# Kernel optimization log

Measured on AMD Instinct MI355X. Metric: run time of the kernel, lower is better.

Reference implementation:

```python
import math
import jax, jax.numpy as jnp
import numpy as np

H = 8
C_HIDDEN = 32
C_Q = 256


def setup_inputs() -> dict:
    key = jax.random.key(0)
    ks = jax.random.split(key, 9)
    B, S, Q, K = 1, 128, 256, 256
    q_x = jax.random.normal(ks[0], (B, S, Q, C_Q), dtype=jnp.float32)
    kv_x = jax.random.normal(ks[1], (B, S, K, C_Q), dtype=jnp.float32)
    bias1 = jax.random.normal(ks[2], (B, S, 1, 1, K), dtype=jnp.float32)
    bias2 = jax.random.normal(ks[3], (B, 1, H, Q, K), dtype=jnp.float32)
    scale = 1.0 / math.sqrt(C_Q)
    wq = jax.random.normal(ks[4], (H * C_HIDDEN, C_Q), dtype=jnp.float32) * scale
    wk = jax.random.normal(ks[5], (H * C_HIDDEN, C_Q), dtype=jnp.float32) * scale
    wv = jax.random.normal(ks[6], (H * C_HIDDEN, C_Q), dtype=jnp.float32) * scale
    wg = jax.random.normal(ks[7], (H * C_HIDDEN, C_Q), dtype=jnp.float32) * scale
    wo = jax.random.normal(ks[8], (C_Q, H * C_HIDDEN), dtype=jnp.float32) * scale
    return {"q_x": q_x, "kv_x": kv_x, "bias1": bias1, "bias2": bias2,
            "wq": wq, "wk": wk, "wv": wv, "wg": wg, "wo": wo}


def _split_heads(x):
    # [..., L, H*c] -> [..., H, L, c]
    y = x.reshape(x.shape[:-1] + (H, C_HIDDEN))
    return jnp.moveaxis(y, -2, -3)


def reference(q_x, kv_x, bias1, bias2, wq, wk, wv, wg, wo):
    # QKV projections (no bias), per-head split, scale q by 1/sqrt(c_hidden)
    q = _split_heads(q_x @ wq.T) / math.sqrt(C_HIDDEN)   # [B,S,H,Q,c]
    k = _split_heads(kv_x @ wk.T)                         # [B,S,H,K,c]
    v = _split_heads(kv_x @ wv.T)                         # [B,S,H,K,c]
    # attention logits with additive biases folded in
    a = jnp.einsum('...hqc,...hkc->...hqk', q, k) + bias1 + bias2
    a = jax.nn.softmax(a, axis=-1)
    o = jnp.einsum('...hqk,...hkc->...hqc', a, v)         # [B,S,H,Q,c]
    o = jnp.moveaxis(o, -3, -2)                           # [B,S,Q,H,c]
    # sigmoid gating from query data
    g = jax.nn.sigmoid(q_x @ wg.T)                        # [B,S,Q,H*c]
    g = g.reshape(g.shape[:-1] + (H, C_HIDDEN))
    o = o * g
    o = o.reshape(o.shape[:-2] + (H * C_HIDDEN,))         # flatten heads
    return o @ wo.T                                       # [B,S,Q,C_Q]
```

## Files before the change

kernel.cpp:

```cpp
#include <hip/hip_runtime.h>
#include <math.h>

#define S_DIM 128
#define H_DIM 8
#define M_TOT (S_DIM * 256)

typedef unsigned short ushort_t;
typedef unsigned int   uint32;
typedef __bf16  v8bf  __attribute__((ext_vector_type(8)));
typedef float   v4f   __attribute__((ext_vector_type(4)));

__device__ inline ushort_t f2b(float x) {
    unsigned int u = __float_as_uint(x);
    u += 0x7fffu + ((u >> 16) & 1u);
    return (ushort_t)(u >> 16);
}
__device__ inline float b2f(ushort_t h) {
    return __uint_as_float(((unsigned int)h) << 16);
}

#define GLDS16(gp, lp) __builtin_amdgcn_global_load_lds( \
    (const __attribute__((address_space(1))) void*)(gp), \
    (__attribute__((address_space(3))) void*)(lp), 16, 0, 0)

__global__ __launch_bounds__(256) void split_x(
    const float* __restrict__ xq, const float* __restrict__ xkv,
    ushort_t* __restrict__ hi, ushort_t* __restrict__ lo)
{
    const size_t BUF4 = (size_t)M_TOT * 64;
    const float* src = blockIdx.y ? xkv : xq;
    size_t base = (size_t)blockIdx.y * BUF4;
    int i = blockIdx.x * 256 + threadIdx.x;
    float4 v = ((const float4*)src)[i];
    ushort4 h, l;
    h.x = f2b(v.x); l.x = f2b(v.x - b2f(h.x));
    h.y = f2b(v.y); l.y = f2b(v.y - b2f(h.y));
    h.z = f2b(v.z); l.z = f2b(v.z - b2f(h.z));
    h.w = f2b(v.w); l.w = f2b(v.w - b2f(h.w));
    ((ushort4*)hi)[base + i] = h;
    ((ushort4*)lo)[base + i] = l;
}

__global__ __launch_bounds__(256) void split_w(
    const float* __restrict__ w0, const float* __restrict__ w1,
    const float* __restrict__ w2, const float* __restrict__ w3,
    const float* __restrict__ w4,
    ushort_t* __restrict__ hi, ushort_t* __restrict__ lo)
{
    const float* src;
    switch (blockIdx.y) {
        case 0: src = w0; break; case 1: src = w1; break;
        case 2: src = w2; break; case 3: src = w3; break;
        default: src = w4; break;
    }
    int i = blockIdx.x * 256 + threadIdx.x;
    float4 v = ((const float4*)src)[i];
    ushort4 h, l;
    h.x = f2b(v.x); l.x = f2b(v.x - b2f(h.x));
    h.y = f2b(v.y); l.y = f2b(v.y - b2f(h.y));
    h.z = f2b(v.z); l.z = f2b(v.z - b2f(h.z));
    h.w = f2b(v.w); l.w = f2b(v.w - b2f(h.w));
    size_t base = (size_t)blockIdx.y * 16384;
    ((ushort4*)hi)[base + i] = h;
    ((ushort4*)lo)[base + i] = l;
}


__global__ __launch_bounds__(256) void gemm_proj(
    const ushort_t* __restrict__ Xhi, const ushort_t* __restrict__ Xlo,
    const ushort_t* __restrict__ Whi4, const ushort_t* __restrict__ Wlo4,
    ushort_t* __restrict__ qh, ushort_t* __restrict__ ql,
    ushort_t* __restrict__ kh, ushort_t* __restrict__ kl,
    float* __restrict__ g_out,
    ushort_t* __restrict__ vh,
    float qscale)
{
    __shared__ ushort_t lds[2][4][128 * 32];

    const int z    = blockIdx.z;
    const int L    = blockIdx.x + 4 * blockIdx.y;
    const int mti  = ((L >> 5) << 3) + (L & 7);
    const int nti  = (L >> 3) & 3;
    const int t    = threadIdx.x;
    const int l    = t & 63;
    const int wv   = t >> 6;
    const int wm   = wv & 1;
    const int wn   = wv >> 1;
    const int idx  = l & 15;
    const int quad = l >> 4;
    const int m0   = mti * 128;
    const int n0   = nti * 128;

    const size_t BUF = (size_t)M_TOT * 256;
    const ushort_t* Ahi = Xhi + (size_t)z * BUF;
    const ushort_t* Alo = Xlo + (size_t)z * BUF;
    const ushort_t* Whi = Whi4 + (size_t)z * 131072;
    const ushort_t* Wlo = Wlo4 + (size_t)z * 131072;
    const float scale = z ? 1.f : qscale;

    const ushort_t* srcs[4] = { Ahi + (size_t)m0 * 256, Alo + (size_t)m0 * 256,
                                Whi + (size_t)n0 * 256, Wlo + (size_t)n0 * 256 };

    size_t stoff[2]; int sdst[2];
    #pragma unroll
    for (int i = 0; i < 2; ++i) {
        const int sb   = wv * 128 + i * 64;
        const int slot = sb + l;
        const int row  = slot >> 2;
        const int gseg = ((slot & 3) - (row >> 1)) & 3;
        stoff[i] = (size_t)row * 256 + gseg * 8;
        sdst[i]  = sb * 8;
    }

    v4f acc[4][4];
    #pragma unroll
    for (int i = 0; i < 4; ++i)
        #pragma unroll
        for (int j = 0; j < 4; ++j) acc[i][j] = (v4f){0.f, 0.f, 0.f, 0.f};

    const int ra  = wm * 64 + 0 * 16 + idx;
    (void)ra;

    #pragma unroll
    for (int b = 0; b < 4; ++b)
        #pragma unroll
        for (int i = 0; i < 2; ++i)
            GLDS16(srcs[b] + stoff[i], &lds[0][b][sdst[i]]);
    __builtin_amdgcn_s_waitcnt(0);
    __syncthreads();

    int cur = 0;
    for (int k0 = 0; k0 < 256; k0 += 32) {
        if (k0 < 224) {
            #pragma unroll
            for (int b = 0; b < 4; ++b)
                #pragma unroll
                for (int i = 0; i < 2; ++i)
                    GLDS16(srcs[b] + stoff[i] + k0 + 32, &lds[cur ^ 1][b][sdst[i]]);
        }

        v8bf ah[4], al[4], bh[4], bl[4];
        #pragma unroll
        for (int mt = 0; mt < 4; ++mt) {
            const int r   = wm * 64 + mt * 16 + idx;
            const int off = r * 32 + (((quad + (r >> 1)) & 3) << 3);
            ah[mt] = *(const v8bf*)&lds[cur][0][off];
            al[mt] = *(const v8bf*)&lds[cur][1][off];
        }
        #pragma unroll
        for (int nt = 0; nt < 4; ++nt) {
            const int r   = wn * 64 + nt * 16 + idx;
            const int off = r * 32 + (((quad + (r >> 1)) & 3) << 3);
            bh[nt] = *(const v8bf*)&lds[cur][2][off];
            bl[nt] = *(const v8bf*)&lds[cur][3][off];
        }

        #pragma unroll
        for (int mt = 0; mt < 4; ++mt)
            #pragma unroll
            for (int nt = 0; nt < 4; ++nt) {
                acc[mt][nt] = __builtin_amdgcn_mfma_f32_16x16x32_bf16(ah[mt], bh[nt], acc[mt][nt], 0, 0, 0);
                acc[mt][nt] = __builtin_amdgcn_mfma_f32_16x16x32_bf16(al[mt], bh[nt], acc[mt][nt], 0, 0, 0);
                acc[mt][nt] = __builtin_amdgcn_mfma_f32_16x16x32_bf16(ah[mt], bl[nt], acc[mt][nt], 0, 0, 0);
            }

        __builtin_amdgcn_s_waitcnt(0);
        __syncthreads();
        cur ^= 1;
    }

    ushort_t* dsth = z ? kh : qh;
    ushort_t* dstl = z ? kl : ql;

    #pragma unroll
    for (int mt = 0; mt < 4; ++mt) {
        const int mbase = m0 + wm * 64 + mt * 16 + quad * 4;
        const int s = mbase >> 8, r8 = mbase & 255;
        #pragma unroll
        for (int nt = 0; nt < 4; ++nt) {
            const int gcol = n0 + wn * 64 + nt * 16 + idx;
            if (gcol < 256) {
                const int hh = gcol >> 5, c = gcol & 31;
                const size_t di = (((size_t)(s * 8 + hh) * 256) + r8) * 32 + c;
                #pragma unroll
                for (int r = 0; r < 4; ++r) {
                    const float val = acc[mt][nt][r] * scale;
                    const ushort_t hv = f2b(val);
                    dsth[di + (size_t)r * 32] = hv;
                    dstl[di + (size_t)r * 32] = f2b(val - b2f(hv));
                }
            } else if (z == 0) {
                const int gc = gcol - 256;
                #pragma unroll
                for (int r = 0; r < 4; ++r)
                    g_out[(size_t)(mbase + r) * 256 + gc] = acc[mt][nt][r];
            } else {
                const int gc = gcol - 256, hh = gc >> 5, c = gc & 31;
                ushort4 hv4;
                #pragma unroll
                for (int r = 0; r < 4; ++r)
                    ((ushort_t*)&hv4)[r] = f2b(acc[mt][nt][r]);
                const size_t di = (((size_t)(s * 8 + hh) * 32) + c) * 256 + r8;
                *(ushort4*)&vh[di] = hv4;
            }
        }
    }
}

__global__ __launch_bounds__(256) void gemm_out(
    const ushort_t* __restrict__ Ah, const ushort_t* __restrict__ Whi,
    const ushort_t* __restrict__ Wlo, float* __restrict__ Cf)
{
    __shared__ ushort_t lds[2][3][128 * 32];

    const int L    = blockIdx.x + 2 * blockIdx.y;
    const int mti  = ((L >> 4) << 3) + (L & 7);
    const int nti  = (L >> 3) & 1;
    const int t    = threadIdx.x;
    const int l    = t & 63;
    const int wv   = t >> 6;
    const int wm   = wv & 1;
    const int wn   = wv >> 1;
    const int idx  = l & 15;
    const int quad = l >> 4;
    const int m0   = mti * 128;
    const int n0   = nti * 128;

    const ushort_t* srcs[3] = { Ah + (size_t)m0 * 256,
                                Whi + (size_t)n0 * 256, Wlo + (size_t)n0 * 256 };

    size_t stoff[2]; int sdst[2];
    #pragma unroll
    for (int i = 0; i < 2; ++i) {
        const int sb   = wv * 128 + i * 64;
        const int slot = sb + l;
        const int row  = slot >> 2;
        const int gseg = ((slot & 3) - (row >> 1)) & 3;
        stoff[i] = (size_t)row * 256 + gseg * 8;
        sdst[i]  = sb * 8;
    }

    v4f acc[4][4];
    #pragma unroll
    for (int i = 0; i < 4; ++i)
        #pragma unroll
        for (int j = 0; j < 4; ++j) acc[i][j] = (v4f){0.f, 0.f, 0.f, 0.f};

    #pragma unroll
    for (int b = 0; b < 3; ++b)
        #pragma unroll
        for (int i = 0; i < 2; ++i)
            GLDS16(srcs[b] + stoff[i], &lds[0][b][sdst[i]]);
    __builtin_amdgcn_s_waitcnt(0);
    __syncthreads();

    int cur = 0;
    for (int k0 = 0; k0 < 256; k0 += 32) {
        if (k0 < 224) {
            #pragma unroll
            for (int b = 0; b < 3; ++b)
                #pragma unroll
                for (int i = 0; i < 2; ++i)
                    GLDS16(srcs[b] + stoff[i] + k0 + 32, &lds[cur ^ 1][b][sdst[i]]);
        }

        v8bf ah[4], bh[4], bl[4];
        #pragma unroll
        for (int mt = 0; mt < 4; ++mt) {
            const int r   = wm * 64 + mt * 16 + idx;
            const int off = r * 32 + (((quad + (r >> 1)) & 3) << 3);
            ah[mt] = *(const v8bf*)&lds[cur][0][off];
        }
        #pragma unroll
        for (int nt = 0; nt < 4; ++nt) {
            const int r   = wn * 64 + nt * 16 + idx;
            const int off = r * 32 + (((quad + (r >> 1)) & 3) << 3);
            bh[nt] = *(const v8bf*)&lds[cur][1][off];
            bl[nt] = *(const v8bf*)&lds[cur][2][off];
        }

        #pragma unroll
        for (int mt = 0; mt < 4; ++mt)
            #pragma unroll
            for (int nt = 0; nt < 4; ++nt) {
                acc[mt][nt] = __builtin_amdgcn_mfma_f32_16x16x32_bf16(ah[mt], bh[nt], acc[mt][nt], 0, 0, 0);
                acc[mt][nt] = __builtin_amdgcn_mfma_f32_16x16x32_bf16(ah[mt], bl[nt], acc[mt][nt], 0, 0, 0);
            }

        __builtin_amdgcn_s_waitcnt(0);
        __syncthreads();
        cur ^= 1;
    }

    #pragma unroll
    for (int mt = 0; mt < 4; ++mt) {
        #pragma unroll
        for (int nt = 0; nt < 4; ++nt) {
            const int gcol = n0 + wn * 64 + nt * 16 + idx;
            #pragma unroll
            for (int r = 0; r < 4; ++r) {
                const int grow = m0 + wm * 64 + mt * 16 + quad * 4 + r;
                Cf[(size_t)grow * 256 + gcol] = acc[mt][nt][r];
            }
        }
    }
}

__global__ __launch_bounds__(256, 2) void attn_mfma(
    const ushort_t* __restrict__ qh, const ushort_t* __restrict__ ql,
    const ushort_t* __restrict__ kh, const ushort_t* __restrict__ kl,
    const ushort_t* __restrict__ vth,
    const float* __restrict__ b1, const float* __restrict__ b2,
    const float* __restrict__ gbuf,
    ushort_t* __restrict__ oh)
{
    __shared__ __align__(16) uint32   pbuf[4][64 * 36];
    __shared__ __align__(16) ushort_t kst[2][3][2048];
    __shared__ __align__(16) float    invl[4][64];

    const int sh = blockIdx.x, s = sh >> 3, h = sh & 7;
    const int t = threadIdx.x, l = t & 63, w = t >> 6;
    const int idx = l & 15, quad = l >> 4;

    const size_t shb = (size_t)sh * 8192;
    const ushort_t* qhp = qh + shb;
    const ushort_t* qlp = ql + shb;
    const ushort_t* khp = kh + shb;
    const ushort_t* klp = kl + shb;
    const ushort_t* vhp = vth + shb;
    const float* b1p = b1 + (size_t)s * 256;
    const float* b2p = b2 + (size_t)h * 65536;

    const int ksrow = t >> 2;
    const int ksseg = ((t & 3) - (ksrow >> 1)) & 3;
    const size_t koff = (size_t)ksrow * 32 + ksseg * 8;
    const int vc   = (t >> 2) & 31;
    const int vkt  = t >> 7;
    const int vseg = ((t & 3) - (vc >> 1)) & 3;
    const size_t voff = (size_t)vc * 256 + vkt * 32 + vseg * 8;
    const int wbase = w * 512;

    v8bf qfh[4], qfl[4];
    #pragma unroll
    for (int nt = 0; nt < 4; ++nt) {
        const int off = (w * 64 + nt * 16 + idx) * 32 + quad * 8;
        qfh[nt] = *(const v8bf*)(qhp + off);
        qfl[nt] = *(const v8bf*)(qlp + off);
    }

    v4f oacc[4][2];
    #pragma unroll
    for (int mt = 0; mt < 4; ++mt) {
        oacc[mt][0] = (v4f){0.f, 0.f, 0.f, 0.f};
        oacc[mt][1] = (v4f){0.f, 0.f, 0.f, 0.f};
    }
    float lrun[4] = {0.f, 0.f, 0.f, 0.f};

    GLDS16(khp + koff, &kst[0][0][wbase]);
    GLDS16(klp + koff, &kst[0][1][wbase]);
    GLDS16(vhp + voff, &kst[0][2][wbase]);
    __builtin_amdgcn_s_waitcnt(0);
    __syncthreads();

    for (int c4 = 0; c4 < 4; ++c4) {
        const int ak0 = c4 * 64;
        const int cur = c4 & 1;

        if (c4 < 3) {
            const size_t nb = (size_t)(ak0 + 64) * 32;
            GLDS16(khp + nb + koff, &kst[cur ^ 1][0][wbase]);
            GLDS16(klp + nb + koff, &kst[cur ^ 1][1][wbase]);
            GLDS16(vhp + (ak0 + 64) + voff, &kst[cur ^ 1][2][wbase]);
        }

        v8bf kfh[4], kfl[4];
        #pragma unroll
        for (int at = 0; at < 4; ++at) {
            const int row = at * 16 + idx;
            const int off = row * 32 + (((quad + (row >> 1)) & 3) << 3);
            kfh[at] = *(const v8bf*)&kst[cur][0][off];
            kfl[at] = *(const v8bf*)&kst[cur][1][off];
        }

        v4f sacc[4][4];
        #pragma unroll
        for (int at = 0; at < 4; ++at)
            #pragma unroll
            for (int nt = 0; nt < 4; ++nt)
                sacc[at][nt] = (v4f){0.f, 0.f, 0.f, 0.f};
        __builtin_amdgcn_s_setprio(1);
        #pragma unroll
        for (int at = 0; at < 4; ++at)
            #pragma unroll
            for (int nt = 0; nt < 4; ++nt) {
                sacc[at][nt] = __builtin_amdgcn_mfma_f32_16x16x32_bf16(kfh[at], qfh[nt], sacc[at][nt], 0, 0, 0);
                sacc[at][nt] = __builtin_amdgcn_mfma_f32_16x16x32_bf16(kfl[at], qfh[nt], sacc[at][nt], 0, 0, 0);
                sacc[at][nt] = __builtin_amdgcn_mfma_f32_16x16x32_bf16(kfh[at], qfl[nt], sacc[at][nt], 0, 0, 0);
            }
        __builtin_amdgcn_s_setprio(0);

        v8bf vfh[2][2];
        #pragma unroll
        for (int n2 = 0; n2 < 2; ++n2)
            #pragma unroll
            for (int kt = 0; kt < 2; ++kt) {
                const int c  = n2 * 16 + idx;
                const int sp = (quad + (c >> 1)) & 3;
                vfh[n2][kt] = *(const v8bf*)&kst[cur][2][kt * 1024 + c * 32 + sp * 8];
            }

        v4f b1v[4];
        #pragma unroll
        for (int at = 0; at < 4; ++at)
            b1v[at] = *(const v4f*)(b1p + ak0 + at * 16 + quad * 4);

        #pragma unroll
        for (int at = 0; at < 4; ++at)
            #pragma unroll
            for (int nt = 0; nt < 4; ++nt) {
                const int q = w * 64 + nt * 16 + idx;
                v4f b2v = *(const v4f*)(b2p + (size_t)q * 256 + ak0 + at * 16 + quad * 4);
                float e0 = __expf(b1v[at][0] + b2v[0] + sacc[at][nt][0]);
                float e1 = __expf(b1v[at][1] + b2v[1] + sacc[at][nt][1]);
                float e2 = __expf(b1v[at][2] + b2v[2] + sacc[at][nt][2]);
                float e3 = __expf(b1v[at][3] + b2v[3] + sacc[at][nt][3]);
                lrun[nt] += (e0 + e1) + (e2 + e3);
                uint32 p0 = __builtin_amdgcn_perm(__float_as_uint(e1) + 0x8000u,
                                                  __float_as_uint(e0) + 0x8000u, 0x07060302u);
                uint32 p1 = __builtin_amdgcn_perm(__float_as_uint(e3) + 0x8000u,
                                                  __float_as_uint(e2) + 0x8000u, 0x07060302u);
                const int dw = (nt * 16 + idx) * 36 + at * 8 + quad * 2;
                *(uint2*)&pbuf[w][dw] = make_uint2(p0, p1);
            }

        __builtin_amdgcn_s_setprio(1);
        #pragma unroll
        for (int mt = 0; mt < 4; ++mt)
            #pragma unroll
            for (int kt = 0; kt < 2; ++kt) {
                v8bf pf = *(const v8bf*)&pbuf[w][(mt * 16 + idx) * 36 + kt * 16 + quad * 4];
                #pragma unroll
                for (int n2 = 0; n2 < 2; ++n2)
                    oacc[mt][n2] = __builtin_amdgcn_mfma_f32_16x16x32_bf16(pf, vfh[n2][kt], oacc[mt][n2], 0, 0, 0);
            }
        __builtin_amdgcn_s_setprio(0);

        __builtin_amdgcn_s_waitcnt(0);
        __syncthreads();
    }

    #pragma unroll
    for (int nt = 0; nt < 4; ++nt) {
        float v = lrun[nt];
        v += __shfl_xor(v, 16, 64);
        v += __shfl_xor(v, 32, 64);
        if (quad == 0) invl[w][nt * 16 + idx] = 1.f / v;
    }

    #pragma unroll
    for (int mt = 0; mt < 4; ++mt) {
        v4f iv = *(const v4f*)&invl[w][mt * 16 + quad * 4];
        #pragma unroll
        for (int n2 = 0; n2 < 2; ++n2) {
            const int c = n2 * 16 + idx;
            #pragma unroll
            for (int r = 0; r < 4; ++r) {
                const int q = w * 64 + mt * 16 + quad * 4 + r;
                const size_t gi = (size_t)(s * 256 + q) * 256 + h * 32 + c;
                const float gv = gbuf[gi];
                const float sig = 1.f / (1.f + __expf(-gv));
                oh[gi] = f2b(oacc[mt][n2][r] * iv[r] * sig);
            }
        }
    }
}

extern "C" void kernel_launch(void* const* d_in, const int* in_sizes, int n_in,
                              void* d_out, int out_size, void* d_ws, size_t ws_size,
                              hipStream_t stream)
{
    const float* q_x   = (const float*)d_in[0];
    const float* kv_x  = (const float*)d_in[1];
    const float* bias1 = (const float*)d_in[2];
    const float* bias2 = (const float*)d_in[3];
    const float* wq    = (const float*)d_in[4];
    const float* wk    = (const float*)d_in[5];
    const float* wv    = (const float*)d_in[6];
    const float* wg    = (const float*)d_in[7];
    const float* wo    = (const float*)d_in[8];
    float* out = (float*)d_out;

    const size_t BUF = (size_t)M_TOT * 256;

    float*    g_buf = (float*)d_ws;
    ushort_t* p     = (ushort_t*)(g_buf + BUF);
    ushort_t* qhb = p;            ushort_t* qlb = qhb + BUF;
    ushort_t* khb = qlb + BUF;    ushort_t* klb = khb + BUF;
    ushort_t* vhb = klb + BUF;
    ushort_t* ohb = vhb + BUF;
    ushort_t* xhb = ohb + BUF;    ushort_t* xlb = xhb + 2 * BUF;
    ushort_t* w_hi = xlb + 2 * BUF;
    ushort_t* w_lo = w_hi + 5 * 65536;

    const float qscale = 0.17677669529663689f;

    split_w<<<dim3(64, 5), 256, 0, stream>>>(wq, wg, wk, wv, wo, w_hi, w_lo);

    split_x<<<dim3(8192, 2), 256, 0, stream>>>(q_x, kv_x, xhb, xlb);

    gemm_proj<<<dim3(4, 256, 2), 256, 0, stream>>>(
        xhb, xlb, w_hi, w_lo, qhb, qlb, khb, klb, g_buf, vhb, qscale);

    attn_mfma<<<S_DIM * H_DIM, 256, 0, stream>>>(
        qhb, qlb, khb, klb, vhb, bias1, bias2, g_buf, ohb);

    gemm_out<<<dim3(2, 256), 256, 0, stream>>>(
        ohb, w_hi + 4 * 65536, w_lo + 4 * 65536, out);
}
```

Before: 264.0 us.

## Fuse fp32 input bf16 hi/lo split into projection GEMM loads

Drops the separate split_x kernel that turned q_x and kv_x into bf16 hi/lo buffers. The projection GEMM now streams fp32 activations straight into LDS and does the hi/lo split on the fly after reading from LDS. This removes one kernel launch and a full write and re-read of the split activation buffers. In exchange the GEMM repeats the conversion work for each N tile, and its A-tile LDS footprint doubles because the data is now fp32.

```diff
diff --git a/kernel.cpp b/kernel.cpp
--- a/kernel.cpp
+++ b/kernel.cpp
@@ -9,6 +9,7 @@
 typedef unsigned int   uint32;
 typedef __bf16  v8bf  __attribute__((ext_vector_type(8)));
 typedef float   v4f   __attribute__((ext_vector_type(4)));
+typedef uint32  u32x4 __attribute__((ext_vector_type(4)));
 
 __device__ inline ushort_t f2b(float x) {
     unsigned int u = __float_as_uint(x);
@@ -19,27 +20,27 @@
     return __uint_as_float(((unsigned int)h) << 16);
 }
 
+__device__ inline uint32 pack2(float e0, float e1) {
+    return __builtin_amdgcn_perm(__float_as_uint(e1) + 0x8000u,
+                                 __float_as_uint(e0) + 0x8000u, 0x07060302u);
+}
+__device__ inline void split_pair(float e0, float e1, uint32& hp, uint32& lp) {
+    hp = pack2(e0, e1);
+    const float h0 = __uint_as_float(hp << 16);
+    const float h1 = __uint_as_float(hp & 0xffff0000u);
+    lp = pack2(e0 - h0, e1 - h1);
+}
+__device__ inline void cvt_split8(v4f a, v4f b, v8bf& h, v8bf& l) {
+    uint32 h0, h1, h2, h3, l0, l1, l2, l3;
+    split_pair(a[0], a[1], h0, l0); split_pair(a[2], a[3], h1, l1);
+    split_pair(b[0], b[1], h2, l2); split_pair(b[2], b[3], h3, l3);
+    u32x4 hp = {h0, h1, h2, h3}, lp = {l0, l1, l2, l3};
+    h = *(v8bf*)&hp; l = *(v8bf*)&lp;
+}
+
 #define GLDS16(gp, lp) __builtin_amdgcn_global_load_lds( \
     (const __attribute__((address_space(1))) void*)(gp), \
     (__attribute__((address_space(3))) void*)(lp), 16, 0, 0)
-
-__global__ __launch_bounds__(256) void split_x(
-    const float* __restrict__ xq, const float* __restrict__ xkv,
-    ushort_t* __restrict__ hi, ushort_t* __restrict__ lo)
-{
-    const size_t BUF4 = (size_t)M_TOT * 64;
-    const float* src = blockIdx.y ? xkv : xq;
-    size_t base = (size_t)blockIdx.y * BUF4;
-    int i = blockIdx.x * 256 + threadIdx.x;
-    float4 v = ((const float4*)src)[i];
-    ushort4 h, l;
-    h.x = f2b(v.x); l.x = f2b(v.x - b2f(h.x));
-    h.y = f2b(v.y); l.y = f2b(v.y - b2f(h.y));
-    h.z = f2b(v.z); l.z = f2b(v.z - b2f(h.z));
-    h.w = f2b(v.w); l.w = f2b(v.w - b2f(h.w));
-    ((ushort4*)hi)[base + i] = h;
-    ((ushort4*)lo)[base + i] = l;
-}
 
 __global__ __launch_bounds__(256) void split_w(
     const float* __restrict__ w0, const float* __restrict__ w1,
@@ -67,7 +68,7 @@
 
 
 __global__ __launch_bounds__(256) void gemm_proj(
-    const ushort_t* __restrict__ Xhi, const ushort_t* __restrict__ Xlo,
+    const float* __restrict__ xq, const float* __restrict__ xkv,
     const ushort_t* __restrict__ Whi4, const ushort_t* __restrict__ Wlo4,
     ushort_t* __restrict__ qh, ushort_t* __restrict__ ql,
     ushort_t* __restrict__ kh, ushort_t* __restrict__ kl,
@@ -75,7 +76,8 @@
     ushort_t* __restrict__ vh,
     float qscale)
 {
-    __shared__ ushort_t lds[2][4][128 * 32];
+    __shared__ float    ldsA[2][4096];
+    __shared__ ushort_t ldsW[2][2][4096];
 
     const int z    = blockIdx.z;
     const int L    = blockIdx.x + 4 * blockIdx.y;
@@ -91,25 +93,28 @@
     const int m0   = mti * 128;
     const int n0   = nti * 128;
 
-    const size_t BUF = (size_t)M_TOT * 256;
-    const ushort_t* Ahi = Xhi + (size_t)z * BUF;
-    const ushort_t* Alo = Xlo + (size_t)z * BUF;
-    const ushort_t* Whi = Whi4 + (size_t)z * 131072;
-    const ushort_t* Wlo = Wlo4 + (size_t)z * 131072;
+    const float* Asrc = (z ? xkv : xq) + (size_t)m0 * 256;
+    const ushort_t* Whi = Whi4 + (size_t)z * 131072 + (size_t)n0 * 256;
+    const ushort_t* Wlo = Wlo4 + (size_t)z * 131072 + (size_t)n0 * 256;
     const float scale = z ? 1.f : qscale;
 
-    const ushort_t* srcs[4] = { Ahi + (size_t)m0 * 256, Alo + (size_t)m0 * 256,
-                                Whi + (size_t)n0 * 256, Wlo + (size_t)n0 * 256 };
-
-    size_t stoff[2]; int sdst[2];
+    size_t stA[4];
+    #pragma unroll
+    for (int j = 0; j < 4; ++j) {
+        const int slot = j * 256 + t;
+        const int c2 = slot >> 9, row = (slot >> 2) & 127, seg = slot & 3;
+        const int gseg = (seg - (row >> 1)) & 3;
+        stA[j] = (size_t)row * 256 + c2 * 16 + gseg * 4;
+    }
+    size_t stW[2]; int sdW[2];
     #pragma unroll
     for (int i = 0; i < 2; ++i) {
         const int sb   = wv * 128 + i * 64;
         const int slot = sb + l;
         const int row  = slot >> 2;
         const int gseg = ((slot & 3) - (row >> 1)) & 3;
-        stoff[i] = (size_t)row * 256 + gseg * 8;
-        sdst[i]  = sb * 8;
+        stW[i] = (size_t)row * 256 + gseg * 8;
+        sdW[i] = sb * 8;
     }
 
     v4f acc[4][4];
@@ -118,41 +123,48 @@
         #pragma unroll
         for (int j = 0; j < 4; ++j) acc[i][j] = (v4f){0.f, 0.f, 0.f, 0.f};
 
-    const int ra  = wm * 64 + 0 * 16 + idx;
-    (void)ra;
-
-    #pragma unroll
-    for (int b = 0; b < 4; ++b)
-        #pragma unroll
-        for (int i = 0; i < 2; ++i)
-            GLDS16(srcs[b] + stoff[i], &lds[0][b][sdst[i]]);
+    #pragma unroll
+    for (int j = 0; j < 4; ++j)
+        GLDS16(Asrc + stA[j], &ldsA[0][(j * 256 + wv * 64) * 4]);
+    #pragma unroll
+    for (int i = 0; i < 2; ++i) {
+        GLDS16(Whi + stW[i], &ldsW[0][0][sdW[i]]);
+        GLDS16(Wlo + stW[i], &ldsW[0][1][sdW[i]]);
+    }
     __builtin_amdgcn_s_waitcnt(0);
     __syncthreads();
+
+    const int c2 = quad >> 1;
+    const int s0 = (quad & 1) * 2;
 
     int cur = 0;
     for (int k0 = 0; k0 < 256; k0 += 32) {
         if (k0 < 224) {
             #pragma unroll
-            for (int b = 0; b < 4; ++b)
-                #pragma unroll
-                for (int i = 0; i < 2; ++i)
-                    GLDS16(srcs[b] + stoff[i] + k0 + 32, &lds[cur ^ 1][b][sdst[i]]);
+            for (int j = 0; j < 4; ++j)
+                GLDS16(Asrc + stA[j] + k0 + 32, &ldsA[cur ^ 1][(j * 256 + wv * 64) * 4]);
+            #pragma unroll
+            for (int i = 0; i < 2; ++i) {
+                GLDS16(Whi + stW[i] + k0 + 32, &ldsW[cur ^ 1][0][sdW[i]]);
+                GLDS16(Wlo + stW[i] + k0 + 32, &ldsW[cur ^ 1][1][sdW[i]]);
+            }
         }
 
         v8bf ah[4], al[4], bh[4], bl[4];
         #pragma unroll
         for (int mt = 0; mt < 4; ++mt) {
-            const int r   = wm * 64 + mt * 16 + idx;
-            const int off = r * 32 + (((quad + (r >> 1)) & 3) << 3);
-            ah[mt] = *(const v8bf*)&lds[cur][0][off];
-            al[mt] = *(const v8bf*)&lds[cur][1][off];
+            const int r  = wm * 64 + mt * 16 + idx;
+            const int rb = c2 * 2048 + r * 16;
+            v4f fa = *(const v4f*)&ldsA[cur][rb + (((s0 + (r >> 1)) & 3) << 2)];
+            v4f fb = *(const v4f*)&ldsA[cur][rb + (((s0 + 1 + (r >> 1)) & 3) << 2)];
+            cvt_split8(fa, fb, ah[mt], al[mt]);
         }
         #pragma unroll
         for (int nt = 0; nt < 4; ++nt) {
             const int r   = wn * 64 + nt * 16 + idx;
             const int off = r * 32 + (((quad + (r >> 1)) & 3) << 3);
-            bh[nt] = *(const v8bf*)&lds[cur][2][off];
-            bl[nt] = *(const v8bf*)&lds[cur][3][off];
+            bh[nt] = *(const v8bf*)&ldsW[cur][0][off];
+            bl[nt] = *(const v8bf*)&ldsW[cur][1][off];
         }
 
         #pragma unroll
@@ -425,10 +437,8 @@
                 float e2 = __expf(b1v[at][2] + b2v[2] + sacc[at][nt][2]);
                 float e3 = __expf(b1v[at][3] + b2v[3] + sacc[at][nt][3]);
                 lrun[nt] += (e0 + e1) + (e2 + e3);
-                uint32 p0 = __builtin_amdgcn_perm(__float_as_uint(e1) + 0x8000u,
-                                                  __float_as_uint(e0) + 0x8000u, 0x07060302u);
-                uint32 p1 = __builtin_amdgcn_perm(__float_as_uint(e3) + 0x8000u,
-                                                  __float_as_uint(e2) + 0x8000u, 0x07060302u);
+                uint32 p0 = pack2(e0, e1);
+                uint32 p1 = pack2(e2, e3);
                 const int dw = (nt * 16 + idx) * 36 + at * 8 + quad * 2;
                 *(uint2*)&pbuf[w][dw] = make_uint2(p0, p1);
             }
@@ -498,18 +508,15 @@
     ushort_t* khb = qlb + BUF;    ushort_t* klb = khb + BUF;
     ushort_t* vhb = klb + BUF;
     ushort_t* ohb = vhb + BUF;
-    ushort_t* xhb = ohb + BUF;    ushort_t* xlb = xhb + 2 * BUF;
-    ushort_t* w_hi = xlb + 2 * BUF;
+    ushort_t* w_hi = ohb + BUF;
     ushort_t* w_lo = w_hi + 5 * 65536;
 
     const float qscale = 0.17677669529663689f;
 
     split_w<<<dim3(64, 5), 256, 0, stream>>>(wq, wg, wk, wv, wo, w_hi, w_lo);
 
-    split_x<<<dim3(8192, 2), 256, 0, stream>>>(q_x, kv_x, xhb, xlb);
-
     gemm_proj<<<dim3(4, 256, 2), 256, 0, stream>>>(
-        xhb, xlb, w_hi, w_lo, qhb, qlb, khb, klb, g_buf, vhb, qscale);
+        q_x, kv_x, w_hi, w_lo, qhb, qlb, khb, klb, g_buf, vhb, qscale);
 
     attn_mfma<<<S_DIM * H_DIM, 256, 0, stream>>>(
         qhb, qlb, khb, klb, vhb, bias1, bias2, g_buf, ohb);
```

Result: no change. 267.7 us (+1.4%).
